# Performance work log

Hardware: AMD Instinct MI355X
Metric: run time of the kernel (lower is better)

The kernel has to match this reference:

```python
import jax, jax.numpy as jnp
import numpy as np

D_IN = 1024
D_OUT = 1024
NUM_HEADS = 16
D_HEAD = D_OUT // NUM_HEADS


def setup_inputs() -> dict:
    key = jax.random.key(0)
    ks = jax.random.split(key, 6)
    s = 0.02
    return {
        "x": jax.random.normal(ks[0], (2, 2048, D_IN), dtype=jnp.float32),
        "W_q": jax.random.normal(ks[1], (D_IN, D_OUT), dtype=jnp.float32) * s,
        "W_k": jax.random.normal(ks[2], (D_IN, D_OUT), dtype=jnp.float32) * s,
        "W_v": jax.random.normal(ks[3], (D_IN, D_OUT), dtype=jnp.float32) * s,
        "W_o": jax.random.normal(ks[4], (D_OUT, D_OUT), dtype=jnp.float32) * s,
        "b_o": jax.random.normal(ks[5], (D_OUT,), dtype=jnp.float32) * s,
    }


def reference(x, W_q, W_k, W_v, W_o, b_o):
    B, T, _ = x.shape
    # qkv projections (no bias), split heads -> [B, H, T, d_head]
    def split_heads(t):
        return t.reshape(B, T, NUM_HEADS, D_HEAD).transpose(0, 2, 1, 3)
    q = split_heads(x @ W_q)
    k = split_heads(x @ W_k)
    v = split_heads(x @ W_v)
    # full causal scores [B, H, T, T]
    scores = jnp.einsum("bhqd,bhkd->bhqk", q, k)
    causal = jnp.triu(jnp.ones((T, T), dtype=bool), k=1)
    scores = jnp.where(causal, -jnp.inf, scores)
    attn = jax.nn.softmax(scores / np.sqrt(D_HEAD).astype(np.float32), axis=-1)
    # dropout rate is 0.0 -> identity
    ctx = jnp.einsum("bhqk,bhkd->bhqd", attn, v)
    ctx = ctx.transpose(0, 2, 1, 3).reshape(B, T, D_OUT)
    return ctx @ W_o + b_o
```

## Files before the change

kernel.cpp:

```cpp
#include <hip/hip_runtime.h>
#include <hip/hip_bf16.h>
#include <cstdint>

#define SEQ_T 2048
#define DMODEL 1024
#define NHEAD 16
#define DHEAD 64

typedef __attribute__((ext_vector_type(8))) __bf16 bf16x8;
typedef __attribute__((ext_vector_type(4))) float floatx4;
typedef __attribute__((ext_vector_type(16))) float floatx16;
typedef __attribute__((ext_vector_type(2))) unsigned uint32x2;

static __device__ __forceinline__ uint16_t f2bf(float f) {
    union { float f; uint32_t u; } v; v.f = f;
    uint32_t r = v.u + 0x7FFFu + ((v.u >> 16) & 1u);
    return (uint16_t)(r >> 16);
}

static __device__ __forceinline__ uint32_t pack2bf(float a, float b) {
    union { __bf16 h[2]; uint32_t u; } p;
    p.h[0] = (__bf16)a; p.h[1] = (__bf16)b;
    return p.u;
}

__global__ void mha_cvt(const float* __restrict__ x, uint16_t* __restrict__ xb,
                        const float* __restrict__ W0, const float* __restrict__ W1,
                        const float* __restrict__ W2, const float* __restrict__ W3,
                        uint16_t* __restrict__ T0, uint16_t* __restrict__ T1,
                        uint16_t* __restrict__ T2, uint16_t* __restrict__ T3) {
    if (blockIdx.z == 4) {
        int base = (blockIdx.y * 16 + blockIdx.x) * 256 + threadIdx.x;
#pragma unroll
        for (int i = 0; i < 16; ++i) {
            int idx = base + i * 65536;
            float4 f = ((const float4*)x)[idx];
            union { uint16_t u[4]; uint64_t v; } o;
            o.u[0] = f2bf(f.x); o.u[1] = f2bf(f.y); o.u[2] = f2bf(f.z); o.u[3] = f2bf(f.w);
            ((uint64_t*)xb)[idx] = o.v;
        }
        return;
    }
    const float* W; uint16_t* Tt; float sc;
    switch (blockIdx.z) {
        case 0: W = W0; Tt = T0; sc = 0.125f * 1.44269504089f; break;
        case 1: W = W1; Tt = T1; sc = 1.f; break;
        case 2: W = W2; Tt = T2; sc = 1.f; break;
        default: W = W3; Tt = T3; sc = 1.f; break;
    }
    __shared__ float tile[64][65];
    const int c  = threadIdx.x & 63;
    const int r0 = threadIdx.x >> 6;
    const int R0 = blockIdx.y * 64, C0 = blockIdx.x * 64;
#pragma unroll
    for (int rr = 0; rr < 16; ++rr) {
        int r = r0 + rr * 4;
        tile[r][c] = W[(size_t)(R0 + r) * DMODEL + C0 + c];
    }
    __syncthreads();
#pragma unroll
    for (int rr = 0; rr < 16; ++rr) {
        int r = r0 + rr * 4;
        Tt[(size_t)(C0 + r) * DMODEL + R0 + c] = f2bf(tile[c][r] * sc);
    }
}

template<int MODE>
__device__ __forceinline__ void gemm_bk64_body(
    const uint16_t* __restrict__ A, const uint16_t* __restrict__ Bt,
    uint16_t* __restrict__ outB) {
    const int K = DMODEL, N = DMODEL;
    extern __shared__ char smem[];
    uint16_t* As = (uint16_t*)smem;
    uint16_t* Bs = (uint16_t*)(smem + 8192);
    const int tid  = threadIdx.x;
    const int wave = tid >> 6;
    const int lane = tid & 63;
    const int m0 = blockIdx.y * 64;
    const int n0 = blockIdx.x * 128;
    const int lr   = lane & 15;
    const int quad = lane >> 4;

    floatx4 acc[4][2];
#pragma unroll
    for (int i = 0; i < 4; ++i)
#pragma unroll
        for (int j = 0; j < 2; ++j) acc[i][j] = (floatx4)0.0f;

    for (int k0 = 0; k0 < K; k0 += 64) {
#pragma unroll
        for (int i = 0; i < 2; ++i) {
            int c = i * 256 + tid;
            int r = c >> 3, s = (c & 7) ^ (r & 7);
            const uint16_t* g = A + (size_t)(m0 + r) * K + k0 + s * 8;
            __builtin_amdgcn_global_load_lds((const __attribute__((address_space(1))) void*)g,
                                             (__attribute__((address_space(3))) void*)(As + (size_t)c * 8), 16, 0, 0);
        }
#pragma unroll
        for (int i = 0; i < 4; ++i) {
            int c = i * 256 + tid;
            int r = c >> 3, s = (c & 7) ^ (r & 7);
            const uint16_t* g = Bt + (size_t)(n0 + r) * K + k0 + s * 8;
            __builtin_amdgcn_global_load_lds((const __attribute__((address_space(1))) void*)g,
                                             (__attribute__((address_space(3))) void*)(Bs + (size_t)c * 8), 16, 0, 0);
        }
        __syncthreads();
#pragma unroll
        for (int ks = 0; ks < 2; ++ks) {
            bf16x8 af[4], bfr[2];
#pragma unroll
            for (int mi = 0; mi < 4; ++mi) {
                int row = mi * 16 + lr;
                af[mi] = *(const bf16x8*)&As[row * 64 + (((ks * 4 + quad) ^ (row & 7)) << 3)];
            }
#pragma unroll
            for (int ni = 0; ni < 2; ++ni) {
                int row = wave * 32 + ni * 16 + lr;
                bfr[ni] = *(const bf16x8*)&Bs[row * 64 + (((ks * 4 + quad) ^ (row & 7)) << 3)];
            }
#pragma unroll
            for (int mi = 0; mi < 4; ++mi)
#pragma unroll
                for (int ni = 0; ni < 2; ++ni)
                    acc[mi][ni] = __builtin_amdgcn_mfma_f32_16x16x32_bf16(af[mi], bfr[ni], acc[mi][ni], 0, 0, 0);
        }
        __syncthreads();
    }
    if constexpr (MODE == 1) {
        uint16_t* Ct = (uint16_t*)smem;
        const int bb = m0 >> 11, t0 = m0 & 2047;
#pragma unroll
        for (int mi = 0; mi < 4; ++mi)
#pragma unroll
            for (int ni = 0; ni < 2; ++ni) {
                int cl = wave * 32 + ni * 16 + lr;
                int tl = mi * 16 + quad * 4;
                int tls = tl ^ ((cl & 3) << 4);
                union { uint16_t u[4]; uint64_t v8; } pk;
#pragma unroll
                for (int r = 0; r < 4; ++r) pk.u[r] = f2bf(acc[mi][ni][r]);
                *(uint64_t*)&Ct[cl * 72 + tls] = pk.v8;
            }
        __syncthreads();
#pragma unroll
        for (int k = 0; k < 4; ++k) {
            int c = k * 256 + tid;
            int cl = c >> 3, off = (c & 7) * 8;
            int offs = off ^ ((cl & 3) << 4);
            uint4 v = *(const uint4*)&Ct[cl * 72 + offs];
            *(uint4*)&outB[((size_t)(bb * 1024 + n0 + cl)) * 2048 + t0 + off] = v;
        }
    } else {
#pragma unroll
        for (int mi = 0; mi < 4; ++mi)
#pragma unroll
            for (int ni = 0; ni < 2; ++ni) {
                int col = n0 + wave * 32 + ni * 16 + lr;
#pragma unroll
                for (int r = 0; r < 4; ++r) {
                    int row = m0 + mi * 16 + quad * 4 + r;
                    outB[(size_t)row * N + col] = f2bf(acc[mi][ni][r]);
                }
            }
    }
}

__global__ __launch_bounds__(256) void mha_gemm_qkv(
    const uint16_t* __restrict__ A,
    const uint16_t* __restrict__ Wq, const uint16_t* __restrict__ Wk, const uint16_t* __restrict__ Wv,
    uint16_t* __restrict__ Q, uint16_t* __restrict__ K, uint16_t* __restrict__ Vt) {
    switch (blockIdx.z) {
        case 0:  gemm_bk64_body<0>(A, Wq, Q);  break;
        case 1:  gemm_bk64_body<0>(A, Wk, K);  break;
        default: gemm_bk64_body<1>(A, Wv, Vt); break;
    }
}

__global__ __launch_bounds__(512) void mha_gemm_out(
    const uint16_t* __restrict__ A, const uint16_t* __restrict__ Wot,
    float* __restrict__ out, const float* __restrict__ bias) {
    const int K = DMODEL, N = DMODEL;
    extern __shared__ char smem[];
    uint16_t* As = (uint16_t*)smem;
    uint16_t* Bs = (uint16_t*)(smem + 8192);
    const int tid  = threadIdx.x;
    const int wave = tid >> 6;
    const int lane = tid & 63;
    const int m0 = blockIdx.y * 64;
    const int n0 = blockIdx.x * 128;
    const int lr   = lane & 15;
    const int quad = lane >> 4;
    const int wm = wave >> 2, wn = wave & 3;

    floatx4 acc[2][2];
#pragma unroll
    for (int i = 0; i < 2; ++i)
#pragma unroll
        for (int j = 0; j < 2; ++j) acc[i][j] = (floatx4)0.0f;

    for (int k0 = 0; k0 < K; k0 += 64) {
        {
            int c = tid;
            int r = c >> 3, s = (c & 7) ^ (r & 7);
            const uint16_t* g = A + (size_t)(m0 + r) * K + k0 + s * 8;
            __builtin_amdgcn_global_load_lds((const __attribute__((address_space(1))) void*)g,
                                             (__attribute__((address_space(3))) void*)(As + (size_t)c * 8), 16, 0, 0);
        }
#pragma unroll
        for (int i = 0; i < 2; ++i) {
            int c = i * 512 + tid;
            int r = c >> 3, s = (c & 7) ^ (r & 7);
            const uint16_t* g = Wot + (size_t)(n0 + r) * K + k0 + s * 8;
            __builtin_amdgcn_global_load_lds((const __attribute__((address_space(1))) void*)g,
                                             (__attribute__((address_space(3))) void*)(Bs + (size_t)c * 8), 16, 0, 0);
        }
        __syncthreads();
#pragma unroll
        for (int ks = 0; ks < 2; ++ks) {
            bf16x8 af[2], bfr[2];
#pragma unroll
            for (int mi = 0; mi < 2; ++mi) {
                int row = wm * 32 + mi * 16 + lr;
                af[mi] = *(const bf16x8*)&As[row * 64 + (((ks * 4 + quad) ^ (row & 7)) << 3)];
            }
#pragma unroll
            for (int ni = 0; ni < 2; ++ni) {
                int row = wn * 32 + ni * 16 + lr;
                bfr[ni] = *(const bf16x8*)&Bs[row * 64 + (((ks * 4 + quad) ^ (row & 7)) << 3)];
            }
#pragma unroll
            for (int mi = 0; mi < 2; ++mi)
#pragma unroll
                for (int ni = 0; ni < 2; ++ni)
                    acc[mi][ni] = __builtin_amdgcn_mfma_f32_16x16x32_bf16(af[mi], bfr[ni], acc[mi][ni], 0, 0, 0);
        }
        __syncthreads();
    }
#pragma unroll
    for (int mi = 0; mi < 2; ++mi)
#pragma unroll
        for (int ni = 0; ni < 2; ++ni) {
            int col = n0 + wn * 32 + ni * 16 + lr;
            float bv = bias[col];
#pragma unroll
            for (int r = 0; r < 4; ++r) {
                int row = m0 + wm * 32 + mi * 16 + quad * 4 + r;
                out[(size_t)row * N + col] = acc[mi][ni][r] + bv;
            }
        }
}

__global__ __launch_bounds__(512, 4) void mha_attn_mfma(
    const uint16_t* __restrict__ Q, const uint16_t* __restrict__ K,
    const uint16_t* __restrict__ Vt, uint16_t* __restrict__ ctx) {
    extern __shared__ char asmem[];
    uint16_t* Ks0 = (uint16_t*)asmem;
    uint16_t* Vs0 = (uint16_t*)(asmem + 32768);

    const int tid  = threadIdx.x;
    const int wave = tid >> 6;
    const int lane = tid & 63;
    const int l31  = lane & 31;
    const int hi   = lane >> 5;
    const int l7   = lane & 7;
    const int qg   = wave & 1;
    const int kvq  = wave >> 1;
    const int h = blockIdx.x;
    const int p = blockIdx.y;
    const int b = blockIdx.z;
    const int jH = 31 - p, jL = p;
    const int TH = (33 - p) >> 1;

    const uint16_t* kg[2];
    const uint16_t* vg[2];
    int cch[2];
#pragma unroll
    for (int i = 0; i < 2; ++i) {
        int c = i * 512 + tid; cch[i] = c;
        int rk = c >> 3, ck = c & 7;
        kg[i] = K + ((size_t)(b * SEQ_T) + rk) * DMODEL + h * DHEAD + ((ck ^ (rk & 7)) * 8);
        int rv = c >> 4, cv = c & 15;
        int sv = (cv & 8) | ((cv & 7) ^ (rv & 7));
        vg[i] = Vt + ((size_t)(b * 1024 + h * DHEAD + rv)) * 2048 + sv * 8;
    }

    int q0w = jH * 64 + qg * 32;
    bf16x8 qf[4];
    auto load_q = [&]() {
        const uint16_t* qb = Q + ((size_t)(b * SEQ_T) + q0w + l31) * DMODEL + h * DHEAD;
#pragma unroll
        for (int f = 0; f < 4; ++f)
            qf[f] = *(const bf16x8*)(qb + f * 16 + hi * 8);
    };
    load_q();

    floatx16 o[2];
#pragma unroll
    for (int dt = 0; dt < 2; ++dt) o[dt] = (floatx16)0.0f;
    float lac = 0.f;

    auto stage = [&](int kv0, int buf) {
        uint16_t* kd = Ks0 + buf * 8192;
        uint16_t* vd = Vs0 + buf * 8192;
#pragma unroll
        for (int i = 0; i < 2; ++i) {
            __builtin_amdgcn_global_load_lds(
                (const __attribute__((address_space(1))) void*)(kg[i] + (size_t)kv0 * DMODEL),
                (__attribute__((address_space(3))) void*)(kd + cch[i] * 8), 16, 0, 0);
            __builtin_amdgcn_global_load_lds(
                (const __attribute__((address_space(1))) void*)(vg[i] + kv0),
                (__attribute__((address_space(3))) void*)(vd + cch[i] * 8), 16, 0, 0);
        }
    };

    auto halfsum = [&](float x) -> float {
#if __has_builtin(__builtin_amdgcn_permlane32_swap)
        uint32x2 r = __builtin_amdgcn_permlane32_swap(__float_as_uint(x), __float_as_uint(x), false, false);
        return __uint_as_float(r.x) + __uint_as_float(r.y);
#else
        return x + __shfl_xor(x, 32, 64);
#endif
    };

    auto combine_store = [&](int cur) {
        __syncthreads();
        float* osc = (float*)(Ks0 + cur * 8192);
        float* lsc = (float*)(Vs0 + cur * 8192);
        float lt = halfsum(lac);
#pragma unroll
        for (int pass = 3; pass >= 1; --pass) {
            if (kvq == pass) {
                if (pass == 3) {
#pragma unroll
                    for (int dt = 0; dt < 2; ++dt)
#pragma unroll
                        for (int r = 0; r < 16; ++r) {
                            int row = (r & 3) + 8 * (r >> 2) + 4 * hi;
                            osc[(qg * 32 + row) * 64 + dt * 32 + l31] = o[dt][r];
                        }
                    if (lane < 32) lsc[qg * 32 + lane] = lt;
                } else {
#pragma unroll
                    for (int dt = 0; dt < 2; ++dt)
#pragma unroll
                        for (int r = 0; r < 16; ++r) {
                            int row = (r & 3) + 8 * (r >> 2) + 4 * hi;
                            osc[(qg * 32 + row) * 64 + dt * 32 + l31] += o[dt][r];
                        }
                    if (lane < 32) lsc[qg * 32 + lane] += lt;
                }
            }
            __syncthreads();
        }
        if (kvq == 0) {
            float ltot = lt + lsc[qg * 32 + l31];
            if (lane < 32) lsc[64 + qg * 32 + lane] = 1.f / ltot;
#pragma unroll
            for (int dt = 0; dt < 2; ++dt)
#pragma unroll
                for (int r = 0; r < 16; ++r) {
                    int row = (r & 3) + 8 * (r >> 2) + 4 * hi;
                    float ov = o[dt][r] + osc[(qg * 32 + row) * 64 + dt * 32 + l31];
                    float li = lsc[64 + qg * 32 + row];
                    size_t addr = ((size_t)(b * SEQ_T) + q0w + row) * DMODEL + h * DHEAD + dt * 32 + l31;
                    ctx[addr] = f2bf(ov * li);
                }
        }
    };

    stage(0, 0);
    __syncthreads();

    for (int t = 0; t < 17; ++t) {
        const int cur = t & 1;
        const int kv0 = (t < TH ? t : t - TH) * 128;
        if (t + 1 < 17) {
            int tn = t + 1;
            stage((tn < TH ? tn : tn - TH) * 128, tn & 1);
        }
        const uint16_t* Kc = Ks0 + cur * 8192;
        const uint16_t* Vc = Vs0 + cur * 8192;
        const int kb = kv0 + kvq * 32;
        floatx16 s = (floatx16)0.0f;
        __builtin_amdgcn_s_setprio(1);
#pragma unroll
        for (int f = 0; f < 4; ++f) {
            bf16x8 kf = *(const bf16x8*)&Kc[(kvq * 32 + l31) * 64 + (((2 * f + hi) ^ l7) << 3)];
            s = __builtin_amdgcn_mfma_f32_32x32x16_bf16(kf, qf[f], s, 0, 0, 0);
        }
        __builtin_amdgcn_s_setprio(0);
        if (kb + 31 > q0w) {
            int qr = q0w + l31;
#pragma unroll
            for (int r = 0; r < 16; ++r) {
                int k = kb + (r & 3) + 8 * (r >> 2) + 4 * hi;
                if (k > qr) s[r] = -3e38f;
            }
        }
        float se[16];
#pragma unroll
        for (int r = 0; r < 16; ++r) {
            se[r] = __builtin_amdgcn_exp2f(s[r]);
            lac += se[r];
        }
        uint32_t d0[2], d1[2], d2[2], d3[2];
#pragma unroll
        for (int i = 0; i < 2; ++i) {
            d0[i] = pack2bf(se[2 * i],      se[2 * i + 1]);
            d1[i] = pack2bf(se[4 + 2 * i],  se[4 + 2 * i + 1]);
            d2[i] = pack2bf(se[8 + 2 * i],  se[8 + 2 * i + 1]);
            d3[i] = pack2bf(se[12 + 2 * i], se[12 + 2 * i + 1]);
        }
        bf16x8 paf[2];
#if __has_builtin(__builtin_amdgcn_permlane32_swap)
        {
            uint32x2 r0 = __builtin_amdgcn_permlane32_swap(d0[0], d1[0], false, false);
            uint32x2 r1 = __builtin_amdgcn_permlane32_swap(d0[1], d1[1], false, false);
            union { uint32_t u[4]; bf16x8 v; } f0;
            f0.u[0] = r0.x; f0.u[1] = r1.x; f0.u[2] = r0.y; f0.u[3] = r1.y;
            paf[0] = f0.v;
            uint32x2 r2 = __builtin_amdgcn_permlane32_swap(d2[0], d3[0], false, false);
            uint32x2 r3 = __builtin_amdgcn_permlane32_swap(d2[1], d3[1], false, false);
            union { uint32_t u[4]; bf16x8 v; } f1;
            f1.u[0] = r2.x; f1.u[1] = r3.x; f1.u[2] = r2.y; f1.u[3] = r3.y;
            paf[1] = f1.v;
        }
#else
        {
            uint32_t s00 = __shfl_xor((int)d0[0], 32, 64), s01 = __shfl_xor((int)d0[1], 32, 64);
            uint32_t s10 = __shfl_xor((int)d1[0], 32, 64), s11 = __shfl_xor((int)d1[1], 32, 64);
            union { uint32_t u[4]; bf16x8 v; } f0;
            f0.u[0] = hi ? s10 : d0[0]; f0.u[1] = hi ? s11 : d0[1];
            f0.u[2] = hi ? d1[0] : s00; f0.u[3] = hi ? d1[1] : s01;
            paf[0] = f0.v;
            uint32_t s20 = __shfl_xor((int)d2[0], 32, 64), s21 = __shfl_xor((int)d2[1], 32, 64);
            uint32_t s30 = __shfl_xor((int)d3[0], 32, 64), s31 = __shfl_xor((int)d3[1], 32, 64);
            union { uint32_t u[4]; bf16x8 v; } f1;
            f1.u[0] = hi ? s30 : d2[0]; f1.u[1] = hi ? s31 : d2[1];
            f1.u[2] = hi ? d3[0] : s20; f1.u[3] = hi ? d3[1] : s21;
            paf[1] = f1.v;
        }
#endif
        __builtin_amdgcn_s_setprio(1);
#pragma unroll
        for (int f = 0; f < 2; ++f)
#pragma unroll
            for (int dt = 0; dt < 2; ++dt) {
                bf16x8 vf = *(const bf16x8*)&Vc[(dt * 32 + l31) * 128 + (((kvq * 4 + 2 * f + hi) ^ l7) << 3)];
                o[dt] = __builtin_amdgcn_mfma_f32_32x32x16_bf16(paf[f], vf, o[dt], 0, 0, 0);
            }
        __builtin_amdgcn_s_setprio(0);
        if (t == TH - 1) {
            combine_store(cur);
            q0w = jL * 64 + qg * 32;
            load_q();
#pragma unroll
            for (int dt = 0; dt < 2; ++dt) o[dt] = (floatx16)0.0f;
            lac = 0.f;
        }
        if (t + 1 < 17) __syncthreads();
    }
    combine_store(0);
}

extern "C" void kernel_launch(void* const* d_in, const int* in_sizes, int n_in,
                              void* d_out, int out_size, void* d_ws, size_t ws_size,
                              hipStream_t stream) {
    const float* x  = (const float*)d_in[0];
    const float* Wq = (const float*)d_in[1];
    const float* Wk = (const float*)d_in[2];
    const float* Wv = (const float*)d_in[3];
    const float* Wo = (const float*)d_in[4];
    const float* bo = (const float*)d_in[5];
    float* out = (float*)d_out;

    char* ws = (char*)d_ws;
    const size_t SZ_X = (size_t)4096 * DMODEL * 2;
    const size_t SZ_W = (size_t)DMODEL * DMODEL * 2;
    size_t off = 0;
    uint16_t* xb  = (uint16_t*)(ws + off); off += SZ_X;
    uint16_t* wqt = (uint16_t*)(ws + off); off += SZ_W;
    uint16_t* wkt = (uint16_t*)(ws + off); off += SZ_W;
    uint16_t* wvt = (uint16_t*)(ws + off); off += SZ_W;
    uint16_t* wot = (uint16_t*)(ws + off); off += SZ_W;
    uint16_t* Qb  = (uint16_t*)(ws + off); off += SZ_X;
    uint16_t* Kb  = (uint16_t*)(ws + off); off += SZ_X;
    uint16_t* Vtb = (uint16_t*)(ws + off); off += SZ_X;
    uint16_t* Cb  = (uint16_t*)(ws + off); off += SZ_X;
    (void)ws_size; (void)in_sizes; (void)n_in; (void)out_size;

    mha_cvt<<<dim3(16, 16, 5), 256, 0, stream>>>(x, xb, Wq, Wk, Wv, Wo, wqt, wkt, wvt, wot);
    mha_gemm_qkv<<<dim3(8, 64, 3), 256, 24576, stream>>>(xb, wqt, wkt, wvt, Qb, Kb, Vtb);
    mha_attn_mfma<<<dim3(NHEAD, 16, 2), 512, 65536, stream>>>(Qb, Kb, Vtb, Cb);
    mha_gemm_out<<<dim3(8, 64), 512, 24576, stream>>>(Cb, wot, out, bo);
}
```

Before: 181.4 us.

## Read V fragments directly from global memory, staging only K in LDS

The attention kernel stops staging V tiles into LDS. Each wave now loads its V MFMA operands straight from global memory (L2/L1), so only K is double-buffered in static shared memory, which roughly halves LDS use per block. The launch-bounds occupancy hint drops from 4 to 2, and the exp2/pack loop is fused to cut register pressure. The risk is higher global-load latency on the PV MFMA path, since these loads are no longer prefetched or overlapped.

New measurement: 204.2 us. 12.6% more time.

```diff
diff --git a/kernel.cpp b/kernel.cpp
--- a/kernel.cpp
+++ b/kernel.cpp
@@ -250,12 +250,11 @@
         }
 }
 
-__global__ __launch_bounds__(512, 4) void mha_attn_mfma(
+__global__ __launch_bounds__(512, 2) void mha_attn_mfma(
     const uint16_t* __restrict__ Q, const uint16_t* __restrict__ K,
     const uint16_t* __restrict__ Vt, uint16_t* __restrict__ ctx) {
-    extern __shared__ char asmem[];
-    uint16_t* Ks0 = (uint16_t*)asmem;
-    uint16_t* Vs0 = (uint16_t*)(asmem + 32768);
+    __shared__ alignas(16) uint16_t Ks[2][128 * 64];
+    __shared__ float lbuf[256];
 
     const int tid  = threadIdx.x;
     const int wave = tid >> 6;
@@ -272,17 +271,14 @@
     const int TH = (33 - p) >> 1;
 
     const uint16_t* kg[2];
-    const uint16_t* vg[2];
     int cch[2];
 #pragma unroll
     for (int i = 0; i < 2; ++i) {
         int c = i * 512 + tid; cch[i] = c;
         int rk = c >> 3, ck = c & 7;
         kg[i] = K + ((size_t)(b * SEQ_T) + rk) * DMODEL + h * DHEAD + ((ck ^ (rk & 7)) * 8);
-        int rv = c >> 4, cv = c & 15;
-        int sv = (cv & 8) | ((cv & 7) ^ (rv & 7));
-        vg[i] = Vt + ((size_t)(b * 1024 + h * DHEAD + rv)) * 2048 + sv * 8;
-    }
+    }
+    const uint16_t* Vg = Vt + ((size_t)(b * 1024 + h * DHEAD)) * 2048;
 
     int q0w = jH * 64 + qg * 32;
     bf16x8 qf[4];
@@ -300,17 +296,11 @@
     float lac = 0.f;
 
     auto stage = [&](int kv0, int buf) {
-        uint16_t* kd = Ks0 + buf * 8192;
-        uint16_t* vd = Vs0 + buf * 8192;
-#pragma unroll
-        for (int i = 0; i < 2; ++i) {
+#pragma unroll
+        for (int i = 0; i < 2; ++i)
             __builtin_amdgcn_global_load_lds(
                 (const __attribute__((address_space(1))) void*)(kg[i] + (size_t)kv0 * DMODEL),
-                (__attribute__((address_space(3))) void*)(kd + cch[i] * 8), 16, 0, 0);
-            __builtin_amdgcn_global_load_lds(
-                (const __attribute__((address_space(1))) void*)(vg[i] + kv0),
-                (__attribute__((address_space(3))) void*)(vd + cch[i] * 8), 16, 0, 0);
-        }
+                (__attribute__((address_space(3))) void*)(&Ks[buf][cch[i] * 8]), 16, 0, 0);
     };
 
     auto halfsum = [&](float x) -> float {
@@ -324,8 +314,7 @@
 
     auto combine_store = [&](int cur) {
         __syncthreads();
-        float* osc = (float*)(Ks0 + cur * 8192);
-        float* lsc = (float*)(Vs0 + cur * 8192);
+        float* osc = (float*)&Ks[cur][0];
         float lt = halfsum(lac);
 #pragma unroll
         for (int pass = 3; pass >= 1; --pass) {
@@ -338,7 +327,7 @@
                             int row = (r & 3) + 8 * (r >> 2) + 4 * hi;
                             osc[(qg * 32 + row) * 64 + dt * 32 + l31] = o[dt][r];
                         }
-                    if (lane < 32) lsc[qg * 32 + lane] = lt;
+                    if (lane < 32) lbuf[qg * 32 + lane] = lt;
                 } else {
 #pragma unroll
                     for (int dt = 0; dt < 2; ++dt)
@@ -347,21 +336,21 @@
                             int row = (r & 3) + 8 * (r >> 2) + 4 * hi;
                             osc[(qg * 32 + row) * 64 + dt * 32 + l31] += o[dt][r];
                         }
-                    if (lane < 32) lsc[qg * 32 + lane] += lt;
+                    if (lane < 32) lbuf[qg * 32 + lane] += lt;
                 }
             }
             __syncthreads();
         }
         if (kvq == 0) {
-            float ltot = lt + lsc[qg * 32 + l31];
-            if (lane < 32) lsc[64 + qg * 32 + lane] = 1.f / ltot;
+            float ltot = lt + lbuf[qg * 32 + l31];
+            if (lane < 32) lbuf[64 + qg * 32 + lane] = 1.f / ltot;
 #pragma unroll
             for (int dt = 0; dt < 2; ++dt)
 #pragma unroll
                 for (int r = 0; r < 16; ++r) {
                     int row = (r & 3) + 8 * (r >> 2) + 4 * hi;
                     float ov = o[dt][r] + osc[(qg * 32 + row) * 64 + dt * 32 + l31];
-                    float li = lsc[64 + qg * 32 + row];
+                    float li = lbuf[64 + qg * 32 + row];
                     size_t addr = ((size_t)(b * SEQ_T) + q0w + row) * DMODEL + h * DHEAD + dt * 32 + l31;
                     ctx[addr] = f2bf(ov * li);
                 }
@@ -378,14 +367,12 @@
             int tn = t + 1;
             stage((tn < TH ? tn : tn - TH) * 128, tn & 1);
         }
-        const uint16_t* Kc = Ks0 + cur * 8192;
-        const uint16_t* Vc = Vs0 + cur * 8192;
         const int kb = kv0 + kvq * 32;
         floatx16 s = (floatx16)0.0f;
         __builtin_amdgcn_s_setprio(1);
 #pragma unroll
         for (int f = 0; f < 4; ++f) {
-            bf16x8 kf = *(const bf16x8*)&Kc[(kvq * 32 + l31) * 64 + (((2 * f + hi) ^ l7) << 3)];
+            bf16x8 kf = *(const bf16x8*)&Ks[cur][(kvq * 32 + l31) * 64 + (((2 * f + hi) ^ l7) << 3)];
             s = __builtin_amdgcn_mfma_f32_32x32x16_bf16(kf, qf[f], s, 0, 0, 0);
         }
         __builtin_amdgcn_s_setprio(0);
@@ -397,19 +384,18 @@
                 if (k > qr) s[r] = -3e38f;
             }
         }
-        float se[16];
-#pragma unroll
-        for (int r = 0; r < 16; ++r) {
-            se[r] = __builtin_amdgcn_exp2f(s[r]);
-            lac += se[r];
-        }
         uint32_t d0[2], d1[2], d2[2], d3[2];
 #pragma unroll
         for (int i = 0; i < 2; ++i) {
-            d0[i] = pack2bf(se[2 * i],      se[2 * i + 1]);
-            d1[i] = pack2bf(se[4 + 2 * i],  se[4 + 2 * i + 1]);
-            d2[i] = pack2bf(se[8 + 2 * i],  se[8 + 2 * i + 1]);
-            d3[i] = pack2bf(se[12 + 2 * i], se[12 + 2 * i + 1]);
+            float a, c2;
+            a = __builtin_amdgcn_exp2f(s[2 * i]);      c2 = __builtin_amdgcn_exp2f(s[2 * i + 1]);
+            lac += a + c2; d0[i] = pack2bf(a, c2);
+            a = __builtin_amdgcn_exp2f(s[4 + 2 * i]);  c2 = __builtin_amdgcn_exp2f(s[4 + 2 * i + 1]);
+            lac += a + c2; d1[i] = pack2bf(a, c2);
+            a = __builtin_amdgcn_exp2f(s[8 + 2 * i]);  c2 = __builtin_amdgcn_exp2f(s[8 + 2 * i + 1]);
+            lac += a + c2; d2[i] = pack2bf(a, c2);
+            a = __builtin_amdgcn_exp2f(s[12 + 2 * i]); c2 = __builtin_amdgcn_exp2f(s[12 + 2 * i + 1]);
+            lac += a + c2; d3[i] = pack2bf(a, c2);
         }
         bf16x8 paf[2];
 #if __has_builtin(__builtin_amdgcn_permlane32_swap)
@@ -446,7 +432,7 @@
         for (int f = 0; f < 2; ++f)
 #pragma unroll
             for (int dt = 0; dt < 2; ++dt) {
-                bf16x8 vf = *(const bf16x8*)&Vc[(dt * 32 + l31) * 128 + (((kvq * 4 + 2 * f + hi) ^ l7) << 3)];
+                bf16x8 vf = *(const bf16x8*)&Vg[(size_t)(dt * 32 + l31) * 2048 + kv0 + ((kvq * 4 + 2 * f + hi) * 8)];
                 o[dt] = __builtin_amdgcn_mfma_f32_32x32x16_bf16(paf[f], vf, o[dt], 0, 0, 0);
             }
         __builtin_amdgcn_s_setprio(0);
@@ -491,6 +477,6 @@
 
     mha_cvt<<<dim3(16, 16, 5), 256, 0, stream>>>(x, xb, Wq, Wk, Wv, Wo, wqt, wkt, wvt, wot);
     mha_gemm_qkv<<<dim3(8, 64, 3), 256, 24576, stream>>>(xb, wqt, wkt, wvt, Qb, Kb, Vtb);
-    mha_attn_mfma<<<dim3(NHEAD, 16, 2), 512, 65536, stream>>>(Qb, Kb, Vtb, Cb);
+    mha_attn_mfma<<<dim3(NHEAD, 16, 2), 512, 0, stream>>>(Qb, Kb, Vtb, Cb);
     mha_gemm_out<<<dim3(8, 64), 512, 24576, stream>>>(Cb, wot, out, bo);
 }
```
